# Performance work log

Hardware: AMD Instinct MI355X
Metric: run time of the kernel (lower is better)

## Reference

```python
import jax, jax.numpy as jnp
import numpy as np

N = 100000
E = 1600000
IN_C = 128
OUT_C = 32
BN_EPS = 1e-5


def setup_inputs() -> dict:
    key = jax.random.key(0)
    k1, k2, k3, k4, k5, k6 = jax.random.split(key, 6)
    x = jax.random.normal(k1, (N, IN_C), dtype=jnp.float32)
    edge_index = jax.random.randint(k2, (2, E), 0, N, dtype=jnp.int64)
    # GCNConv linear weight (glorot-ish) and bias
    W = jax.random.normal(k3, (IN_C, OUT_C), dtype=jnp.float32) / np.sqrt(IN_C)
    b = jax.random.normal(k4, (OUT_C,), dtype=jnp.float32) * 0.01
    # BatchNorm1d affine params
    gamma = jnp.ones((OUT_C,), dtype=jnp.float32) + 0.1 * jax.random.normal(k5, (OUT_C,), dtype=jnp.float32)
    beta = 0.1 * jax.random.normal(k6, (OUT_C,), dtype=jnp.float32)
    return {"x": x, "edge_index": edge_index, "W": W, "b": b, "gamma": gamma, "beta": beta}


def reference(x, edge_index, W, b, gamma, beta):
    # --- GCNConv (PyG semantics): add self-loops, sym degree norm, linear ---
    self_loops = jnp.arange(N, dtype=edge_index.dtype)
    row = jnp.concatenate([edge_index[0], self_loops])  # source nodes [E+N]
    col = jnp.concatenate([edge_index[1], self_loops])  # target nodes [E+N]

    deg = jax.ops.segment_sum(jnp.ones_like(col, dtype=x.dtype), col, num_segments=N)
    deg_inv_sqrt = jnp.where(deg > 0, jax.lax.rsqrt(deg), 0.0)
    norm = deg_inv_sqrt[row] * deg_inv_sqrt[col]  # [E+N]

    h = x @ W  # project first (PyG order): [N, OUT_C]
    msgs = norm[:, None] * h[row]  # gather + scale: [E+N, OUT_C]
    out = jax.ops.segment_sum(msgs, col, num_segments=N) + b  # scatter-add

    # --- BatchNorm1d (training mode: batch statistics, biased variance) ---
    mean = jnp.mean(out, axis=0)
    var = jnp.mean((out - mean) ** 2, axis=0)
    y = (out - mean) * jax.lax.rsqrt(var + BN_EPS) * gamma + beta
    return y
```

## Files before the change

kernel.cpp:

```cpp
#include <hip/hip_runtime.h>
#include <hip/hip_fp16.h>

#define IN_C  128
#define OUT_C 32
#define BN_EPS 1e-5f
#define BKT_BITS 7
#define BKT 128
#define C_CAP 2816
#define CH  6144

typedef float floatx4 __attribute__((ext_vector_type(4)));

__global__ void zero_kernel(int* __restrict__ bcnt, float* __restrict__ sums) {
    int i = threadIdx.x;
    if (i < 1024) bcnt[i] = 0;
    if (i < 512) sums[i] = 0.0f;
}

__global__ __launch_bounds__(512) void binfill_kernel(
    const int* __restrict__ row, const int* __restrict__ col,
    int* __restrict__ bcnt, int* __restrict__ adjp, int E)
{
    __shared__ int pk[CH];
    __shared__ unsigned short bk[CH];
    __shared__ int h[1024];
    __shared__ int excl[1024];
    __shared__ int lcur[1024];
    __shared__ int basg[1024];
    __shared__ int wsum[8];
    const int t  = threadIdx.x;
    const int e0 = blockIdx.x * CH;
    const int n  = min(CH, E - e0);

    for (int i = t; i < 1024; i += 512) h[i] = 0;
    __syncthreads();

    int myb[12], myp[12];
    #pragma unroll
    for (int k = 0; k < 12; ++k) {
        int i = t + 512 * k;
        myb[k] = -1;
        if (i < n) {
            int c = col[e0 + i];
            int r = row[e0 + i];
            myb[k] = c >> BKT_BITS;
            myp[k] = (r << BKT_BITS) | (c & (BKT - 1));
            atomicAdd(&h[myb[k]], 1);
        }
    }
    __syncthreads();

    {
        const int lane = t & 63;
        int a  = h[2 * t];
        int b2 = h[2 * t + 1];
        int s = a + b2;
        int incl = s;
        #pragma unroll
        for (int d = 1; d < 64; d <<= 1) {
            int u = __shfl_up(incl, d);
            if (lane >= d) incl += u;
        }
        if (lane == 63) wsum[t >> 6] = incl;
        __syncthreads();
        int wpre = 0;
        #pragma unroll
        for (int w = 0; w < 7; ++w) wpre += (w < (t >> 6)) ? wsum[w] : 0;
        int pre = wpre + incl - s;

        excl[2 * t] = pre;          lcur[2 * t] = pre;
        excl[2 * t + 1] = pre + a;  lcur[2 * t + 1] = pre + a;
        int g0 = 0, g1 = 0;
        if (a)  { g0 = atomicAdd(&bcnt[2 * t], a);      if (g0 > C_CAP - a)  g0 = max(0, C_CAP - a); }
        if (b2) { g1 = atomicAdd(&bcnt[2 * t + 1], b2); if (g1 > C_CAP - b2) g1 = max(0, C_CAP - b2); }
        basg[2 * t]     = (2 * t) * C_CAP + g0;
        basg[2 * t + 1] = (2 * t + 1) * C_CAP + g1;
    }
    __syncthreads();

    #pragma unroll
    for (int k = 0; k < 12; ++k) {
        if (myb[k] >= 0) {
            int b = myb[k];
            int l = atomicAdd(&lcur[b], 1);
            pk[l] = myp[k];
            bk[l] = (unsigned short)b;
        }
    }
    __syncthreads();

    for (int i = t; i < n; i += 512) {
        int b = bk[i];
        adjp[basg[b] + (i - excl[b])] = pk[i];
    }
}

__global__ __launch_bounds__(256) void sort_kernel(
    const int* __restrict__ bcnt, int* __restrict__ adjp,
    int* __restrict__ counts, int2* __restrict__ ord2, int N)
{
    __shared__ int eL[C_CAP];
    __shared__ int h[BKT];
    __shared__ int cur[BKT];
    __shared__ int wdeg[BKT];
    __shared__ int eoff[BKT];
    __shared__ int wv[2];
    const int t = threadIdx.x;
    const int b = blockIdx.x;
    const int s0  = b * C_CAP;
    const int cnt = min(bcnt[b], C_CAP);
    const int base = b << BKT_BITS;

    if (t < BKT) h[t] = 0;
    __syncthreads();
    for (int i = t; i < cnt; i += 256) {
        int p = adjp[s0 + i];
        eL[i] = p;
        atomicAdd(&h[p & (BKT - 1)], 1);
    }
    __syncthreads();

    if (t < BKT) {
        const int lane = t & 63;
        int v = h[t];
        int incl = v;
        #pragma unroll
        for (int d = 1; d < 64; d <<= 1) {
            int u = __shfl_up(incl, d);
            if (lane >= d) incl += u;
        }
        if (lane == 63) wv[t >> 6] = incl;
        int e = incl - v;
        eoff[t] = e;
    }
    __syncthreads();
    if (t < BKT) {
        int e = eoff[t] + ((t >= 64) ? wv[0] : 0);
        eoff[t] = e;
        cur[t] = e;
        int nd = base + t;
        if (nd < N) counts[nd] = h[t];
        wdeg[t] = (nd < N) ? h[t] : -1;
    }
    __syncthreads();

    if (t < BKT) {
        int w0 = t & ~31;
        int my = wdeg[t];
        int rank = 0;
        #pragma unroll
        for (int j = 0; j < 32; ++j) {
            int dj = wdeg[w0 + j];
            rank += (dj < my) || (dj == my && (w0 + j) < t);
        }
        int slot = base + w0 + rank;
        if (my >= 0) {
            unsigned pack = ((unsigned)(s0 + eoff[t]) << 8) | (unsigned)min(h[t], 255);
            ord2[slot] = make_int2((int)pack, base + t);
        } else {
            ord2[slot] = make_int2(0, -1);
        }
    }
    __syncthreads();

    for (int i = t; i < cnt; i += 256) {
        int p = eL[i];
        int pos = atomicAdd(&cur[p & (BKT - 1)], 1);
        adjp[s0 + pos] = p >> BKT_BITS;
    }
}

__global__ __launch_bounds__(256) void gemm_kernel(
    const float* __restrict__ x, const float* __restrict__ W,
    const int* __restrict__ counts, __half* __restrict__ gh0,
    __half* __restrict__ gh1, int N)
{
    __shared__ float xs[32 * 132];
    __shared__ float wl[128 * 32];
    const int tid = threadIdx.x;
    const int r0  = blockIdx.x * 32;

    #pragma unroll
    for (int k = 0; k < 4; ++k) {
        int idx = tid + 256 * k;
        int row = idx >> 5;
        int c4  = idx & 31;
        int rr  = r0 + row;
        float4 v = make_float4(0.f, 0.f, 0.f, 0.f);
        if (rr < N) v = reinterpret_cast<const float4*>(x)[(size_t)rr * 32 + c4];
        *reinterpret_cast<float4*>(&xs[row * 132 + c4 * 4]) = v;
    }
    #pragma unroll
    for (int k = 0; k < 4; ++k) {
        int idx = tid + 256 * k;
        reinterpret_cast<float4*>(wl)[idx] = reinterpret_cast<const float4*>(W)[idx];
    }
    __syncthreads();

    const int r_local = tid >> 3;
    const int c4 = (tid & 7) * 4;
    float4 sum = make_float4(0.f, 0.f, 0.f, 0.f);
    #pragma unroll 8
    for (int k = 0; k < 128; ++k) {
        float  xv = xs[r_local * 132 + k];
        float4 w4 = *reinterpret_cast<const float4*>(&wl[k * 32 + c4]);
        sum.x = fmaf(xv, w4.x, sum.x);
        sum.y = fmaf(xv, w4.y, sum.y);
        sum.z = fmaf(xv, w4.z, sum.z);
        sum.w = fmaf(xv, w4.w, sum.w);
    }
    const int r = r0 + r_local;
    if (r < N) {
        float dis = rsqrtf((float)counts[r] + 1.0f);
        union { __half2 h[2]; float2 f; } u;
        u.h[0] = __floats2half2_rn(sum.x * dis, sum.y * dis);
        u.h[1] = __floats2half2_rn(sum.z * dis, sum.w * dis);
        __half* tb = (c4 < 16) ? gh0 : gh1;
        reinterpret_cast<float2*>(tb)[(size_t)r * 4 + ((c4 & 15) >> 2)] = u.f;
    }
}

__global__ __launch_bounds__(256) void pull_kernel(
    const int2* __restrict__ ord2, const int* __restrict__ adjp,
    const __half* __restrict__ gh0, const __half* __restrict__ gh1,
    const float* __restrict__ bias, float* __restrict__ out,
    float* __restrict__ sums, int NW)
{
    const int xcd  = blockIdx.x & 7;
    const int half = xcd >> 2;
    const int stride = (gridDim.x >> 3) * 4;

    __shared__ float4 r1[256];
    __shared__ float4 r2[256];
    const int t   = threadIdx.x;
    const int grp = t >> 4;
    const int way = (t >> 2) & 3;
    const int l4  = t & 3;
    const int chan_off = half * 16;
    const float2* g2 = reinterpret_cast<const float2*>(half ? gh1 : gh0);
    const float4 bc = *reinterpret_cast<const float4*>(&bias[chan_off + l4 * 4]);

    float4 ls = make_float4(0.f, 0.f, 0.f, 0.f);
    float4 lq = make_float4(0.f, 0.f, 0.f, 0.f);

    for (int idx = (blockIdx.x >> 3) * 4 + (xcd & 3); idx < NW; idx += stride) {
        const int2 o0 = ord2[idx * 32 + grp];
        const int2 o1 = ord2[idx * 32 + 31 - grp];
        const int n0 = o0.y, n1 = o1.y;
        const unsigned q0 = (unsigned)o0.x, q1 = (unsigned)o1.x;
        const int len0 = (int)(q0 & 255u);
        const int s0   = (int)(q0 >> 8);
        const int len1 = (int)(q1 & 255u);
        const int s1   = (int)(q1 >> 8);
        const int total = len0 + len1;
        const int s1m = s1 - len0;

        float a00 = 0.f, a01 = 0.f, a02 = 0.f, a03 = 0.f;
        float a10 = 0.f, a11 = 0.f, a12 = 0.f, a13 = 0.f;
        if (way == 0 && n0 >= 0) {
            float2 raw = g2[(size_t)n0 * 4 + l4];
            __half2 p = *reinterpret_cast<__half2*>(&raw.x);
            __half2 q = *reinterpret_cast<__half2*>(&raw.y);
            float2 xx = __half22float2(p), yy = __half22float2(q);
            a00 = xx.x; a01 = xx.y; a02 = yy.x; a03 = yy.y;
        } else if (way == 1 && n1 >= 0) {
            float2 raw = g2[(size_t)n1 * 4 + l4];
            __half2 p = *reinterpret_cast<__half2*>(&raw.x);
            __half2 q = *reinterpret_cast<__half2*>(&raw.y);
            float2 xx = __half22float2(p), yy = __half22float2(q);
            a10 = xx.x; a11 = xx.y; a12 = yy.x; a13 = yy.y;
        }

        #define LDI(kk) __builtin_nontemporal_load(&adjp[(((kk) < len0) ? s0 : s1m) + (kk)])
        #define ACC2(w, s) { \
            __half2 p = *reinterpret_cast<__half2*>(&(w).x); \
            __half2 q = *reinterpret_cast<__half2*>(&(w).y); \
            float2 xx = __half22float2(p), yy = __half22float2(q); \
            a00 += (s) ? xx.x : 0.f;  a10 += (s) ? 0.f : xx.x; \
            a01 += (s) ? xx.y : 0.f;  a11 += (s) ? 0.f : xx.y; \
            a02 += (s) ? yy.x : 0.f;  a12 += (s) ? 0.f : yy.x; \
            a03 += (s) ? yy.y : 0.f;  a13 += (s) ? 0.f : yy.y; }

        int k = way;
        for (; k + 28 < total; k += 32) {
            int e0 = LDI(k);
            int e1 = LDI(k + 4);
            int e2 = LDI(k + 8);
            int e3 = LDI(k + 12);
            int e4 = LDI(k + 16);
            int e5 = LDI(k + 20);
            int e6 = LDI(k + 24);
            int e7 = LDI(k + 28);
            float2 w0 = g2[(size_t)e0 * 4 + l4];
            float2 w1 = g2[(size_t)e1 * 4 + l4];
            float2 w2 = g2[(size_t)e2 * 4 + l4];
            float2 w3 = g2[(size_t)e3 * 4 + l4];
            float2 w4 = g2[(size_t)e4 * 4 + l4];
            float2 w5 = g2[(size_t)e5 * 4 + l4];
            float2 w6 = g2[(size_t)e6 * 4 + l4];
            float2 w7 = g2[(size_t)e7 * 4 + l4];
            ACC2(w0, k      < len0) ACC2(w1, k + 4  < len0)
            ACC2(w2, k + 8  < len0) ACC2(w3, k + 12 < len0)
            ACC2(w4, k + 16 < len0) ACC2(w5, k + 20 < len0)
            ACC2(w6, k + 24 < len0) ACC2(w7, k + 28 < len0)
        }
        for (; k + 12 < total; k += 16) {
            int e0 = LDI(k);
            int e1 = LDI(k + 4);
            int e2 = LDI(k + 8);
            int e3 = LDI(k + 12);
            float2 w0 = g2[(size_t)e0 * 4 + l4];
            float2 w1 = g2[(size_t)e1 * 4 + l4];
            float2 w2 = g2[(size_t)e2 * 4 + l4];
            float2 w3 = g2[(size_t)e3 * 4 + l4];
            ACC2(w0, k      < len0) ACC2(w1, k + 4  < len0)
            ACC2(w2, k + 8  < len0) ACC2(w3, k + 12 < len0)
        }
        for (; k < total; k += 4) {
            int e0 = LDI(k);
            float2 w0 = g2[(size_t)e0 * 4 + l4];
            ACC2(w0, k < len0)
        }
        #undef ACC2
        #undef LDI

        a00 += __shfl_xor(a00, 4); a00 += __shfl_xor(a00, 8);
        a01 += __shfl_xor(a01, 4); a01 += __shfl_xor(a01, 8);
        a02 += __shfl_xor(a02, 4); a02 += __shfl_xor(a02, 8);
        a03 += __shfl_xor(a03, 4); a03 += __shfl_xor(a03, 8);
        a10 += __shfl_xor(a10, 4); a10 += __shfl_xor(a10, 8);
        a11 += __shfl_xor(a11, 4); a11 += __shfl_xor(a11, 8);
        a12 += __shfl_xor(a12, 4); a12 += __shfl_xor(a12, 8);
        a13 += __shfl_xor(a13, 4); a13 += __shfl_xor(a13, 8);

        if (way == 0 && n0 >= 0) {
            float dis = rsqrtf((float)len0 + 1.0f);
            floatx4 v;
            v.x = fmaf(dis, a00, bc.x);
            v.y = fmaf(dis, a01, bc.y);
            v.z = fmaf(dis, a02, bc.z);
            v.w = fmaf(dis, a03, bc.w);
            __builtin_nontemporal_store(v, &reinterpret_cast<floatx4*>(out)[(size_t)n0 * 8 + (chan_off >> 2) + l4]);
            ls.x += v.x; ls.y += v.y; ls.z += v.z; ls.w += v.w;
            lq.x = fmaf(v.x, v.x, lq.x); lq.y = fmaf(v.y, v.y, lq.y);
            lq.z = fmaf(v.z, v.z, lq.z); lq.w = fmaf(v.w, v.w, lq.w);
        } else if (way == 1 && n1 >= 0) {
            float dis = rsqrtf((float)len1 + 1.0f);
            floatx4 v;
            v.x = fmaf(dis, a10, bc.x);
            v.y = fmaf(dis, a11, bc.y);
            v.z = fmaf(dis, a12, bc.z);
            v.w = fmaf(dis, a13, bc.w);
            __builtin_nontemporal_store(v, &reinterpret_cast<floatx4*>(out)[(size_t)n1 * 8 + (chan_off >> 2) + l4]);
            ls.x += v.x; ls.y += v.y; ls.z += v.z; ls.w += v.w;
            lq.x = fmaf(v.x, v.x, lq.x); lq.y = fmaf(v.y, v.y, lq.y);
            lq.z = fmaf(v.z, v.z, lq.z); lq.w = fmaf(v.w, v.w, lq.w);
        }
    }

    r1[t] = ls; r2[t] = lq;
    __syncthreads();
    #pragma unroll
    for (int off = 128; off >= 4; off >>= 1) {
        if (t < off) {
            float4 u1 = r1[t + off], u2 = r2[t + off];
            float4 v1 = r1[t],       v2 = r2[t];
            v1.x += u1.x; v1.y += u1.y; v1.z += u1.z; v1.w += u1.w;
            v2.x += u2.x; v2.y += u2.y; v2.z += u2.z; v2.w += u2.w;
            r1[t] = v1; r2[t] = v2;
        }
        __syncthreads();
    }
    if (t < 4) {
        float4 v1 = r1[t], v2 = r2[t];
        float* sb = sums + (blockIdx.x & 7) * 64;
        int cb = chan_off + 4 * t;
        atomicAdd(&sb[cb + 0], v1.x); atomicAdd(&sb[cb + 1], v1.y);
        atomicAdd(&sb[cb + 2], v1.z); atomicAdd(&sb[cb + 3], v1.w);
        atomicAdd(&sb[32 + cb + 0], v2.x); atomicAdd(&sb[32 + cb + 1], v2.y);
        atomicAdd(&sb[32 + cb + 2], v2.z); atomicAdd(&sb[32 + cb + 3], v2.w);
    }
}

__global__ __launch_bounds__(256) void bn_apply_kernel(
    float* __restrict__ out, const float* __restrict__ sums,
    const float* __restrict__ gamma, const float* __restrict__ beta,
    int N, long long n4)
{
    __shared__ float ssl[64];
    const int t = threadIdx.x;
    if (t < 32) {
        float s = 0.f, q = 0.f;
        #pragma unroll
        for (int r = 0; r < 8; ++r) { s += sums[r * 64 + t]; q += sums[r * 64 + 32 + t]; }
        float invN  = 1.0f / (float)N;
        float mean  = s * invN;
        float var   = q * invN - mean * mean;
        float scale = gamma[t] * rsqrtf(var + BN_EPS);
        ssl[t]      = scale;
        ssl[32 + t] = fmaf(-mean, scale, beta[t]);
    }
    __syncthreads();

    long long i = (long long)blockIdx.x * blockDim.x + t;
    if (i < n4) {
        int c4 = (int)(i & 7) * 4;
        float4 v = reinterpret_cast<float4*>(out)[i];
        v.x = fmaf(v.x, ssl[c4 + 0], ssl[32 + c4 + 0]);
        v.y = fmaf(v.y, ssl[c4 + 1], ssl[32 + c4 + 1]);
        v.z = fmaf(v.z, ssl[c4 + 2], ssl[32 + c4 + 2]);
        v.w = fmaf(v.w, ssl[c4 + 3], ssl[32 + c4 + 3]);
        reinterpret_cast<float4*>(out)[i] = v;
    }
}

extern "C" void kernel_launch(void* const* d_in, const int* in_sizes, int n_in,
                              void* d_out, int out_size, void* d_ws, size_t ws_size,
                              hipStream_t stream)
{
    const float* x     = (const float*)d_in[0];
    const int*   ei    = (const int*)d_in[1];
    const float* W     = (const float*)d_in[2];
    const float* b     = (const float*)d_in[3];
    const float* gamma = (const float*)d_in[4];
    const float* beta  = (const float*)d_in[5];
    float* out = (float*)d_out;

    const int N = in_sizes[0] / IN_C;
    const int E = in_sizes[1] / 2;
    const int* row = ei;
    const int* col = ei + E;
    const int NB = (N + BKT - 1) >> BKT_BITS;

    __half* gh0   = (__half*)d_ws;
    __half* gh1   = gh0 + (size_t)N * 16;
    float* sums   = (float*)(gh1 + (size_t)N * 16);
    int*   counts = (int*)(sums + 576);
    int*   bcnt   = counts + N;
    int2*  ord2   = (int2*)(bcnt + 1024);
    int*   adjp   = (int*)(ord2 + (size_t)NB * BKT);

    zero_kernel   <<<1, 1024, 0, stream>>>(bcnt, sums);
    binfill_kernel<<<(E + CH - 1) / CH, 512, 0, stream>>>(row, col, bcnt, adjp, E);
    sort_kernel   <<<NB, 256, 0, stream>>>(bcnt, adjp, counts, ord2, N);

    gemm_kernel   <<<(N + 31) / 32, 256, 0, stream>>>(x, W, counts, gh0, gh1, N);

    const int NW   = NB * 4;
    pull_kernel   <<<2048, 256, 0, stream>>>(ord2, adjp, gh0, gh1, b, out, sums, NW);

    long long n4 = (long long)N * OUT_C / 4;
    bn_apply_kernel<<<(int)((n4 + 255) / 256), 256, 0, stream>>>(out, sums, gamma, beta, N, n4);
}
```

Measured before the change: 121.0 us.

## Widen pull gather to 8 channels per lane, split BN stats into separate kernel

The pull kernel now has each lane load a float4 of eight half channels instead of a float2 of four, handles two windows per iteration, drops the 32-wide unroll and adds an occupancy hint. Bias addition and the BN statistics accumulation are removed from the pull kernel. A new stats kernel rereads the output to compute sums, on the basis that the bias cancels under batch normalization. The aim is fewer, wider gather loads and lower register and LDS pressure in the hot kernel, at the cost of an extra pass over the output and one more launch.

```diff
diff --git a/kernel.cpp b/kernel.cpp
--- a/kernel.cpp
+++ b/kernel.cpp
@@ -220,148 +220,137 @@
     }
 }
 
-__global__ __launch_bounds__(256) void pull_kernel(
+__global__ __launch_bounds__(256, 8) void pull_kernel(
     const int2* __restrict__ ord2, const int* __restrict__ adjp,
     const __half* __restrict__ gh0, const __half* __restrict__ gh1,
-    const float* __restrict__ bias, float* __restrict__ out,
-    float* __restrict__ sums, int NW)
+    float* __restrict__ out, int NW)
 {
     const int xcd  = blockIdx.x & 7;
     const int half = xcd >> 2;
     const int stride = (gridDim.x >> 3) * 4;
 
-    __shared__ float4 r1[256];
-    __shared__ float4 r2[256];
     const int t   = threadIdx.x;
-    const int grp = t >> 4;
-    const int way = (t >> 2) & 3;
-    const int l4  = t & 3;
-    const int chan_off = half * 16;
-    const float2* g2 = reinterpret_cast<const float2*>(half ? gh1 : gh0);
-    const float4 bc = *reinterpret_cast<const float4*>(&bias[chan_off + l4 * 4]);
-
-    float4 ls = make_float4(0.f, 0.f, 0.f, 0.f);
-    float4 lq = make_float4(0.f, 0.f, 0.f, 0.f);
-
-    for (int idx = (blockIdx.x >> 3) * 4 + (xcd & 3); idx < NW; idx += stride) {
-        const int2 o0 = ord2[idx * 32 + grp];
-        const int2 o1 = ord2[idx * 32 + 31 - grp];
+    const int grp = t >> 3;
+    const int way = (t >> 1) & 3;
+    const int cl  = t & 1;
+    const float4* g4 = reinterpret_cast<const float4*>(half ? gh1 : gh0);
+
+    const int NWP = (NW + 1) >> 1;
+    for (int idx = (blockIdx.x >> 3) * 4 + (xcd & 3); idx < NWP; idx += stride) {
+        const int win = idx * 2 + (grp >> 4);
+        if (win >= NW) continue;
+        const int q = grp & 15;
+        const int2 o0 = ord2[win * 32 + q];
+        const int2 o1 = ord2[win * 32 + 31 - q];
         const int n0 = o0.y, n1 = o1.y;
-        const unsigned q0 = (unsigned)o0.x, q1 = (unsigned)o1.x;
-        const int len0 = (int)(q0 & 255u);
-        const int s0   = (int)(q0 >> 8);
-        const int len1 = (int)(q1 & 255u);
-        const int s1   = (int)(q1 >> 8);
+        const unsigned p0 = (unsigned)o0.x, p1 = (unsigned)o1.x;
+        const int len0 = (int)(p0 & 255u), s0 = (int)(p0 >> 8);
+        const int len1 = (int)(p1 & 255u), s1 = (int)(p1 >> 8);
         const int total = len0 + len1;
         const int s1m = s1 - len0;
 
-        float a00 = 0.f, a01 = 0.f, a02 = 0.f, a03 = 0.f;
-        float a10 = 0.f, a11 = 0.f, a12 = 0.f, a13 = 0.f;
+        float a00=0.f,a01=0.f,a02=0.f,a03=0.f,a04=0.f,a05=0.f,a06=0.f,a07=0.f;
+        float a10=0.f,a11=0.f,a12=0.f,a13=0.f,a14=0.f,a15=0.f,a16=0.f,a17=0.f;
+
+        #define UNPK(Vv) \
+            __half2 h0 = *reinterpret_cast<const __half2*>(&(Vv).x); \
+            __half2 h1 = *reinterpret_cast<const __half2*>(&(Vv).y); \
+            __half2 h2 = *reinterpret_cast<const __half2*>(&(Vv).z); \
+            __half2 h3 = *reinterpret_cast<const __half2*>(&(Vv).w); \
+            float2 u0 = __half22float2(h0), u1 = __half22float2(h1); \
+            float2 u2 = __half22float2(h2), u3 = __half22float2(h3); \
+            float f0 = u0.x, f1 = u0.y, f2 = u1.x, f3 = u1.y; \
+            float f4 = u2.x, f5 = u2.y, f6 = u3.x, f7 = u3.y;
+
         if (way == 0 && n0 >= 0) {
-            float2 raw = g2[(size_t)n0 * 4 + l4];
-            __half2 p = *reinterpret_cast<__half2*>(&raw.x);
-            __half2 q = *reinterpret_cast<__half2*>(&raw.y);
-            float2 xx = __half22float2(p), yy = __half22float2(q);
-            a00 = xx.x; a01 = xx.y; a02 = yy.x; a03 = yy.y;
+            float4 sv = g4[(size_t)n0 * 2 + cl];
+            UNPK(sv)
+            a00=f0; a01=f1; a02=f2; a03=f3; a04=f4; a05=f5; a06=f6; a07=f7;
         } else if (way == 1 && n1 >= 0) {
-            float2 raw = g2[(size_t)n1 * 4 + l4];
-            __half2 p = *reinterpret_cast<__half2*>(&raw.x);
-            __half2 q = *reinterpret_cast<__half2*>(&raw.y);
-            float2 xx = __half22float2(p), yy = __half22float2(q);
-            a10 = xx.x; a11 = xx.y; a12 = yy.x; a13 = yy.y;
+            float4 sv = g4[(size_t)n1 * 2 + cl];
+            UNPK(sv)
+            a10=f0; a11=f1; a12=f2; a13=f3; a14=f4; a15=f5; a16=f6; a17=f7;
         }
 
         #define LDI(kk) __builtin_nontemporal_load(&adjp[(((kk) < len0) ? s0 : s1m) + (kk)])
-        #define ACC2(w, s) { \
-            __half2 p = *reinterpret_cast<__half2*>(&(w).x); \
-            __half2 q = *reinterpret_cast<__half2*>(&(w).y); \
-            float2 xx = __half22float2(p), yy = __half22float2(q); \
-            a00 += (s) ? xx.x : 0.f;  a10 += (s) ? 0.f : xx.x; \
-            a01 += (s) ? xx.y : 0.f;  a11 += (s) ? 0.f : xx.y; \
-            a02 += (s) ? yy.x : 0.f;  a12 += (s) ? 0.f : yy.x; \
-            a03 += (s) ? yy.y : 0.f;  a13 += (s) ? 0.f : yy.y; }
+        #define ACC2(Vv, s) { \
+            UNPK(Vv) \
+            a00 += (s) ? f0 : 0.f;  a10 += (s) ? 0.f : f0; \
+            a01 += (s) ? f1 : 0.f;  a11 += (s) ? 0.f : f1; \
+            a02 += (s) ? f2 : 0.f;  a12 += (s) ? 0.f : f2; \
+            a03 += (s) ? f3 : 0.f;  a13 += (s) ? 0.f : f3; \
+            a04 += (s) ? f4 : 0.f;  a14 += (s) ? 0.f : f4; \
+            a05 += (s) ? f5 : 0.f;  a15 += (s) ? 0.f : f5; \
+            a06 += (s) ? f6 : 0.f;  a16 += (s) ? 0.f : f6; \
+            a07 += (s) ? f7 : 0.f;  a17 += (s) ? 0.f : f7; }
 
         int k = way;
-        for (; k + 28 < total; k += 32) {
-            int e0 = LDI(k);
-            int e1 = LDI(k + 4);
-            int e2 = LDI(k + 8);
-            int e3 = LDI(k + 12);
-            int e4 = LDI(k + 16);
-            int e5 = LDI(k + 20);
-            int e6 = LDI(k + 24);
-            int e7 = LDI(k + 28);
-            float2 w0 = g2[(size_t)e0 * 4 + l4];
-            float2 w1 = g2[(size_t)e1 * 4 + l4];
-            float2 w2 = g2[(size_t)e2 * 4 + l4];
-            float2 w3 = g2[(size_t)e3 * 4 + l4];
-            float2 w4 = g2[(size_t)e4 * 4 + l4];
-            float2 w5 = g2[(size_t)e5 * 4 + l4];
-            float2 w6 = g2[(size_t)e6 * 4 + l4];
-            float2 w7 = g2[(size_t)e7 * 4 + l4];
-            ACC2(w0, k      < len0) ACC2(w1, k + 4  < len0)
-            ACC2(w2, k + 8  < len0) ACC2(w3, k + 12 < len0)
-            ACC2(w4, k + 16 < len0) ACC2(w5, k + 20 < len0)
-            ACC2(w6, k + 24 < len0) ACC2(w7, k + 28 < len0)
-        }
         for (; k + 12 < total; k += 16) {
             int e0 = LDI(k);
             int e1 = LDI(k + 4);
             int e2 = LDI(k + 8);
             int e3 = LDI(k + 12);
-            float2 w0 = g2[(size_t)e0 * 4 + l4];
-            float2 w1 = g2[(size_t)e1 * 4 + l4];
-            float2 w2 = g2[(size_t)e2 * 4 + l4];
-            float2 w3 = g2[(size_t)e3 * 4 + l4];
-            ACC2(w0, k      < len0) ACC2(w1, k + 4  < len0)
-            ACC2(w2, k + 8  < len0) ACC2(w3, k + 12 < len0)
+            float4 w0 = g4[(size_t)e0 * 2 + cl];
+            float4 w1 = g4[(size_t)e1 * 2 + cl];
+            float4 w2 = g4[(size_t)e2 * 2 + cl];
+            float4 w3 = g4[(size_t)e3 * 2 + cl];
+            { ACC2(w0, k      < len0) }
+            { ACC2(w1, k + 4  < len0) }
+            { ACC2(w2, k + 8  < len0) }
+            { ACC2(w3, k + 12 < len0) }
         }
         for (; k < total; k += 4) {
             int e0 = LDI(k);
-            float2 w0 = g2[(size_t)e0 * 4 + l4];
-            ACC2(w0, k < len0)
+            float4 w0 = g4[(size_t)e0 * 2 + cl];
+            { ACC2(w0, k < len0) }
         }
         #undef ACC2
         #undef LDI
-
-        a00 += __shfl_xor(a00, 4); a00 += __shfl_xor(a00, 8);
-        a01 += __shfl_xor(a01, 4); a01 += __shfl_xor(a01, 8);
-        a02 += __shfl_xor(a02, 4); a02 += __shfl_xor(a02, 8);
-        a03 += __shfl_xor(a03, 4); a03 += __shfl_xor(a03, 8);
-        a10 += __shfl_xor(a10, 4); a10 += __shfl_xor(a10, 8);
-        a11 += __shfl_xor(a11, 4); a11 += __shfl_xor(a11, 8);
-        a12 += __shfl_xor(a12, 4); a12 += __shfl_xor(a12, 8);
-        a13 += __shfl_xor(a13, 4); a13 += __shfl_xor(a13, 8);
+        #undef UNPK
+
+        #define RED(a) a += __shfl_xor(a, 2); a += __shfl_xor(a, 4);
+        RED(a00) RED(a01) RED(a02) RED(a03) RED(a04) RED(a05) RED(a06) RED(a07)
+        RED(a10) RED(a11) RED(a12) RED(a13) RED(a14) RED(a15) RED(a16) RED(a17)
+        #undef RED
 
         if (way == 0 && n0 >= 0) {
             float dis = rsqrtf((float)len0 + 1.0f);
-            floatx4 v;
-            v.x = fmaf(dis, a00, bc.x);
-            v.y = fmaf(dis, a01, bc.y);
-            v.z = fmaf(dis, a02, bc.z);
-            v.w = fmaf(dis, a03, bc.w);
-            __builtin_nontemporal_store(v, &reinterpret_cast<floatx4*>(out)[(size_t)n0 * 8 + (chan_off >> 2) + l4]);
-            ls.x += v.x; ls.y += v.y; ls.z += v.z; ls.w += v.w;
-            lq.x = fmaf(v.x, v.x, lq.x); lq.y = fmaf(v.y, v.y, lq.y);
-            lq.z = fmaf(v.z, v.z, lq.z); lq.w = fmaf(v.w, v.w, lq.w);
+            floatx4 v0, v1;
+            v0.x = a00 * dis; v0.y = a01 * dis; v0.z = a02 * dis; v0.w = a03 * dis;
+            v1.x = a04 * dis; v1.y = a05 * dis; v1.z = a06 * dis; v1.w = a07 * dis;
+            size_t ob = (size_t)n0 * 8 + half * 4 + cl * 2;
+            __builtin_nontemporal_store(v0, &reinterpret_cast<floatx4*>(out)[ob]);
+            __builtin_nontemporal_store(v1, &reinterpret_cast<floatx4*>(out)[ob + 1]);
         } else if (way == 1 && n1 >= 0) {
             float dis = rsqrtf((float)len1 + 1.0f);
-            floatx4 v;
-            v.x = fmaf(dis, a10, bc.x);
-            v.y = fmaf(dis, a11, bc.y);
-            v.z = fmaf(dis, a12, bc.z);
-            v.w = fmaf(dis, a13, bc.w);
-            __builtin_nontemporal_store(v, &reinterpret_cast<floatx4*>(out)[(size_t)n1 * 8 + (chan_off >> 2) + l4]);
-            ls.x += v.x; ls.y += v.y; ls.z += v.z; ls.w += v.w;
-            lq.x = fmaf(v.x, v.x, lq.x); lq.y = fmaf(v.y, v.y, lq.y);
-            lq.z = fmaf(v.z, v.z, lq.z); lq.w = fmaf(v.w, v.w, lq.w);
-        }
-    }
-
+            floatx4 v0, v1;
+            v0.x = a10 * dis; v0.y = a11 * dis; v0.z = a12 * dis; v0.w = a13 * dis;
+            v1.x = a14 * dis; v1.y = a15 * dis; v1.z = a16 * dis; v1.w = a17 * dis;
+            size_t ob = (size_t)n1 * 8 + half * 4 + cl * 2;
+            __builtin_nontemporal_store(v0, &reinterpret_cast<floatx4*>(out)[ob]);
+            __builtin_nontemporal_store(v1, &reinterpret_cast<floatx4*>(out)[ob + 1]);
+        }
+    }
+}
+
+__global__ __launch_bounds__(256) void stats_kernel(
+    const float* __restrict__ out, float* __restrict__ sums, long long n4)
+{
+    __shared__ float4 r1[256];
+    __shared__ float4 r2[256];
+    const int t = threadIdx.x;
+    float4 ls = make_float4(0.f, 0.f, 0.f, 0.f);
+    float4 lq = make_float4(0.f, 0.f, 0.f, 0.f);
+    for (long long i = (long long)blockIdx.x * 256 + t; i < n4; i += (long long)gridDim.x * 256) {
+        float4 v = reinterpret_cast<const float4*>(out)[i];
+        ls.x += v.x; ls.y += v.y; ls.z += v.z; ls.w += v.w;
+        lq.x = fmaf(v.x, v.x, lq.x); lq.y = fmaf(v.y, v.y, lq.y);
+        lq.z = fmaf(v.z, v.z, lq.z); lq.w = fmaf(v.w, v.w, lq.w);
+    }
     r1[t] = ls; r2[t] = lq;
     __syncthreads();
     #pragma unroll
-    for (int off = 128; off >= 4; off >>= 1) {
+    for (int off = 128; off >= 8; off >>= 1) {
         if (t < off) {
             float4 u1 = r1[t + off], u2 = r2[t + off];
             float4 v1 = r1[t],       v2 = r2[t];
@@ -371,10 +360,10 @@
         }
         __syncthreads();
     }
-    if (t < 4) {
+    if (t < 8) {
         float4 v1 = r1[t], v2 = r2[t];
         float* sb = sums + (blockIdx.x & 7) * 64;
-        int cb = chan_off + 4 * t;
+        int cb = t * 4;
         atomicAdd(&sb[cb + 0], v1.x); atomicAdd(&sb[cb + 1], v1.y);
         atomicAdd(&sb[cb + 2], v1.z); atomicAdd(&sb[cb + 3], v1.w);
         atomicAdd(&sb[32 + cb + 0], v2.x); atomicAdd(&sb[32 + cb + 1], v2.y);
@@ -421,7 +410,6 @@
     const float* x     = (const float*)d_in[0];
     const int*   ei    = (const int*)d_in[1];
     const float* W     = (const float*)d_in[2];
-    const float* b     = (const float*)d_in[3];
     const float* gamma = (const float*)d_in[4];
     const float* beta  = (const float*)d_in[5];
     float* out = (float*)d_out;
@@ -446,9 +434,10 @@
 
     gemm_kernel   <<<(N + 31) / 32, 256, 0, stream>>>(x, W, counts, gh0, gh1, N);
 
-    const int NW   = NB * 4;
-    pull_kernel   <<<2048, 256, 0, stream>>>(ord2, adjp, gh0, gh1, b, out, sums, NW);
+    const int NW = NB * 4;
+    pull_kernel   <<<2048, 256, 0, stream>>>(ord2, adjp, gh0, gh1, out, NW);
 
     long long n4 = (long long)N * OUT_C / 4;
+    stats_kernel  <<<1024, 256, 0, stream>>>(out, sums, n4);
     bn_apply_kernel<<<(int)((n4 + 255) / 256), 256, 0, stream>>>(out, sums, gamma, beta, N, n4);
 }
```

New measurement: 125.6 us. 3.9% more time.
